# Optimization experiments

Measured on AMD Instinct MI355X. Metric: run time of the kernel, lower is better.

The kernel has to match this reference:

```python
import jax, jax.numpy as jnp
import numpy as np

N = 50000          # total residues (nodes)
E = 800000         # contact edges, avg degree 16
F_IN = 1280        # ESM embedding dim
H = 256            # hidden
L = 4              # num_layers
B = 100            # proteins in batch
MAX_NODES = 500    # residues per protein (uniform -> static to_dense_batch shape)


def setup_inputs() -> dict:
    key = jax.random.key(0)
    ks = jax.random.split(key, 16)
    s = 0.02
    inp = {
        "seq": jax.random.randint(ks[0], (N,), 0, 26),
        "edge_index": jax.random.randint(ks[1], (2, E), 0, N),
        "esm_token": jax.random.normal(ks[2], (N, F_IN), jnp.float32),
        "batch": jnp.arange(N) // MAX_NODES,
        # lin0
        "lin0_W": jax.random.normal(ks[3], (F_IN, H), jnp.float32) * s,
        "lin0_b": jnp.zeros((H,), jnp.float32),
        # WeightConv1 per layer: lin1 (root), lin2 (neighbor), lin3 (mask head)
        "wc_W1": jax.random.normal(ks[4], (L, H, H), jnp.float32) * s,
        "wc_b1": jnp.zeros((L, H), jnp.float32),
        "wc_W2": jax.random.normal(ks[5], (L, H, H), jnp.float32) * s,
        "wc_b2": jnp.zeros((L, H), jnp.float32),
        "wc_W3": jax.random.normal(ks[6], (L, H, H), jnp.float32) * s,
        "wc_b3": jnp.zeros((L, H), jnp.float32),
        # SparseConv per layer: neighbor weight + bias, root weight
        "sc_Wn": jax.random.normal(ks[7], (L, H, H), jnp.float32) * s,
        "sc_bn": jnp.zeros((L, H), jnp.float32),
        "sc_Wr": jax.random.normal(ks[8], (L, H, H), jnp.float32) * s,
    }
    return inp


def reference(seq, edge_index, esm_token, batch,
              lin0_W, lin0_b,
              wc_W1, wc_b1, wc_W2, wc_b2, wc_W3, wc_b3,
              sc_Wn, sc_bn, sc_Wr):
    src, dst = edge_index[0], edge_index[1]
    x = esm_token @ lin0_W + lin0_b              # [N, H]
    mask_val = None
    xs = []
    for i in range(L):
        # ---- WeightConv1: learned edge-conditioned node mask ----
        xm = x if mask_val is None else x * mask_val
        h_nb = xm @ wc_W2[i] + wc_b2[i]          # neighbor transform [N, H]
        agg = jax.ops.segment_sum(h_nb[src], dst, num_segments=N)
        h = jax.nn.relu(agg + xm @ wc_W1[i] + wc_b1[i])
        mask_val = jax.nn.sigmoid(h @ wc_W3[i] + wc_b3[i])   # [N, H]
        # ---- SparseConv: mask-gated sparse aggregation ----
        xg = x * mask_val
        agg2 = jax.ops.segment_sum(xg[src], dst, num_segments=N)
        x = jax.nn.relu(agg2 @ sc_Wn[i] + sc_bn[i] + x @ sc_Wr[i])
        xs.append(x)
    feat = jnp.concatenate(xs, axis=-1)          # jumping-knowledge cat [N, L*H]
    # ---- to_dense_batch ----
    counts = jax.ops.segment_sum(jnp.ones((N,), jnp.int32), batch, num_segments=B)
    starts = jnp.cumsum(counts) - counts
    pos = jnp.arange(N) - starts[batch]
    dense = jnp.zeros((B, MAX_NODES, L * H), feat.dtype).at[batch, pos].set(feat)
    node_mask = jnp.zeros((B, MAX_NODES), bool).at[batch, pos].set(True)
    return dense, node_mask
```

## Files before the change

### kernel.cpp

```cpp
#include <hip/hip_runtime.h>

#define NNODES 50000
#define HDIM 256
#define NLAYERS 4
#define NEDGES 800000
#define FIN 1280
#define LDOUT 1024

typedef _Float16 f16;
typedef __attribute__((ext_vector_type(8))) _Float16 f16x8;
typedef __attribute__((ext_vector_type(4))) _Float16 f16x4;
typedef __attribute__((ext_vector_type(4))) float f32x4;


__global__ __launch_bounds__(256) void hm_k(
    const f16*  __restrict__ aggx,
    const f16*  __restrict__ xm,
    const f16*  __restrict__ xh,
    const int*  __restrict__ deg,
    const f16*  __restrict__ WH,
    const f16*  __restrict__ W3t,
    const float* __restrict__ b2,
    const float* __restrict__ b1,
    const float* __restrict__ b3,
    f16* __restrict__ maskh,
    f16* __restrict__ xg)
{
    __shared__ f16 Hfr[16384];

    const int row0 = blockIdx.x * 64;
    const int tid = threadIdx.x;
    const int wv = tid >> 6;
    const int l = tid & 63;
    const int ak = (l >> 4) * 8;

    int arow[4]; bool av[4];
    #pragma unroll
    for (int rf = 0; rf < 4; ++rf) {
        arow[rf] = row0 + rf * 16 + (l & 15);
        av[rf] = arow[rf] < NNODES;
    }

    const f16* bp[4];
    #pragma unroll
    for (int cf = 0; cf < 4; ++cf)
        bp[cf] = WH + (size_t)(wv * 64 + cf * 16 + (l & 15)) * 512 + ak;

    f32x4 acc[4][4] = {};

    #pragma unroll
    for (int kt = 0; kt < 8; ++kt) {
        const f16* base = (kt < 4) ? aggx : xm;
        const int koff = (kt & 3) * 64 + ak;
        f16x8 af[4][2];
        #pragma unroll
        for (int rf = 0; rf < 4; ++rf)
            #pragma unroll
            for (int kb = 0; kb < 2; ++kb) {
                f16x8 v;
                #pragma unroll
                for (int i = 0; i < 8; ++i) v[i] = (f16)0.f;
                if (av[rf])
                    v = *(const f16x8*)(base + (size_t)arow[rf] * HDIM + koff + kb * 32);
                af[rf][kb] = v;
            }
        f16x8 bf[4][2];
        #pragma unroll
        for (int cf = 0; cf < 4; ++cf) {
            bf[cf][0] = *(const f16x8*)(bp[cf] + kt * 64);
            bf[cf][1] = *(const f16x8*)(bp[cf] + kt * 64 + 32);
        }
        #pragma unroll
        for (int cf = 0; cf < 4; ++cf)
            #pragma unroll
            for (int rf = 0; rf < 4; ++rf)
                #pragma unroll
                for (int kb = 0; kb < 2; ++kb)
                    acc[rf][cf] = __builtin_amdgcn_mfma_f32_16x16x32_f16(
                        af[rf][kb], bf[cf][kb], acc[rf][cf], 0, 0, 0);
    }

    #pragma unroll
    for (int rf = 0; rf < 4; ++rf) {
        #pragma unroll
        for (int j = 0; j < 4; ++j) {
            const int rowl = rf * 16 + ((l >> 4) * 4) + j;
            const int row = row0 + rowl;
            const float dv = (row < NNODES) ? (float)deg[row] : 0.f;
            #pragma unroll
            for (int cf = 0; cf < 4; ++cf) {
                const int col = wv * 64 + cf * 16 + (l & 15);
                const float h = fmaxf(acc[rf][cf][j] + dv * b2[col] + b1[col], 0.f);
                const int idx =
                    (((col >> 6) * 8 + ((col >> 5) & 1) * 4 + (rowl >> 4)) * 64
                     + ((col >> 3) & 3) * 16 + (rowl & 15)) * 8 + (col & 7);
                Hfr[idx] = (f16)h;
            }
        }
    }
    __syncthreads();

    const f16* bp3[4];
    #pragma unroll
    for (int cf = 0; cf < 4; ++cf)
        bp3[cf] = W3t + (size_t)(wv * 64 + cf * 16 + (l & 15)) * 256 + ak;

    f32x4 acc2[4][4] = {};
    #pragma unroll
    for (int kt = 0; kt < 4; ++kt) {
        f16x8 af[4][2];
        #pragma unroll
        for (int rf = 0; rf < 4; ++rf)
            #pragma unroll
            for (int kb = 0; kb < 2; ++kb)
                af[rf][kb] = *(const f16x8*)(&Hfr[((kt * 8 + kb * 4 + rf) * 64 + l) * 8]);
        f16x8 bf[4][2];
        #pragma unroll
        for (int cf = 0; cf < 4; ++cf) {
            bf[cf][0] = *(const f16x8*)(bp3[cf] + kt * 64);
            bf[cf][1] = *(const f16x8*)(bp3[cf] + kt * 64 + 32);
        }
        #pragma unroll
        for (int cf = 0; cf < 4; ++cf)
            #pragma unroll
            for (int rf = 0; rf < 4; ++rf)
                #pragma unroll
                for (int kb = 0; kb < 2; ++kb)
                    acc2[rf][cf] = __builtin_amdgcn_mfma_f32_16x16x32_f16(
                        af[rf][kb], bf[cf][kb], acc2[rf][cf], 0, 0, 0);
    }

    #pragma unroll
    for (int rf = 0; rf < 4; ++rf) {
        #pragma unroll
        for (int j = 0; j < 4; ++j) {
            const int row = row0 + rf * 16 + ((l >> 4) * 4) + j;
            if (row >= NNODES) continue;
            #pragma unroll
            for (int cf = 0; cf < 4; ++cf) {
                const int col = wv * 64 + cf * 16 + (l & 15);
                const float m = 1.f / (1.f + expf(-(acc2[rf][cf][j] + b3[col])));
                maskh[(size_t)row * HDIM + col] = (f16)m;
                xg[(size_t)row * HDIM + col] =
                    (f16)((float)xh[(size_t)row * HDIM + col] * m);
            }
        }
    }
}

__global__ __launch_bounds__(256) void cath2_k(
    const f16*  __restrict__ agg2,
    const f16*  __restrict__ xh,
    const f16*  __restrict__ Mh,
    const f16*  __restrict__ Wt,
    const float* __restrict__ bias,
    float* __restrict__ Cf, int ldc,
    f16*  __restrict__ Ch,
    f16*  __restrict__ Ch3)
{
    const int row0 = blockIdx.x * 64;
    const int tid = threadIdx.x;
    const int wv = tid >> 6;
    const int l = tid & 63;
    const int ak = (l >> 4) * 8;

    int arow[4]; bool av[4];
    #pragma unroll
    for (int rf = 0; rf < 4; ++rf) {
        arow[rf] = row0 + rf * 16 + (l & 15);
        av[rf] = arow[rf] < NNODES;
    }

    const f16* bp[4];
    #pragma unroll
    for (int cf = 0; cf < 4; ++cf)
        bp[cf] = Wt + (size_t)(wv * 64 + cf * 16 + (l & 15)) * 512 + ak;

    f32x4 acc[4][4] = {};

    #pragma unroll
    for (int kt = 0; kt < 8; ++kt) {
        const f16* base = (kt < 4) ? agg2 : xh;
        const int koff = (kt & 3) * 64 + ak;
        f16x8 af[4][2];
        #pragma unroll
        for (int rf = 0; rf < 4; ++rf)
            #pragma unroll
            for (int kb = 0; kb < 2; ++kb) {
                f16x8 v;
                #pragma unroll
                for (int i = 0; i < 8; ++i) v[i] = (f16)0.f;
                if (av[rf])
                    v = *(const f16x8*)(base + (size_t)arow[rf] * HDIM + koff + kb * 32);
                af[rf][kb] = v;
            }
        f16x8 bf[4][2];
        #pragma unroll
        for (int cf = 0; cf < 4; ++cf) {
            bf[cf][0] = *(const f16x8*)(bp[cf] + kt * 64);
            bf[cf][1] = *(const f16x8*)(bp[cf] + kt * 64 + 32);
        }
        #pragma unroll
        for (int cf = 0; cf < 4; ++cf)
            #pragma unroll
            for (int rf = 0; rf < 4; ++rf)
                #pragma unroll
                for (int kb = 0; kb < 2; ++kb)
                    acc[rf][cf] = __builtin_amdgcn_mfma_f32_16x16x32_f16(
                        af[rf][kb], bf[cf][kb], acc[rf][cf], 0, 0, 0);
    }

    __syncthreads();

    #pragma unroll
    for (int rf = 0; rf < 4; ++rf) {
        #pragma unroll
        for (int j = 0; j < 4; ++j) {
            const int row = row0 + rf * 16 + ((l >> 4) * 4) + j;
            if (row >= NNODES) continue;
            #pragma unroll
            for (int cf = 0; cf < 4; ++cf) {
                const int col = wv * 64 + cf * 16 + (l & 15);
                const float r = fmaxf(acc[rf][cf][j] + bias[col], 0.f);
                Cf[(size_t)row * ldc + col] = r;
                Ch[(size_t)row * HDIM + col] = (f16)r;
                Ch3[(size_t)row * HDIM + col] =
                    (f16)(r * (float)Mh[(size_t)row * HDIM + col]);
            }
        }
    }
}

template<int KTILES>
__global__ __launch_bounds__(256) void lin0_k(
    const float* __restrict__ A1, int lda1,
    const f16*  __restrict__ WtBase,
    f16* __restrict__ parts)
{
    constexpr int K = KTILES * 64;
    __shared__ f16 Asm[2][4096];

    const int row0 = blockIdx.x * 64;
    const int by = blockIdx.y;
    const int tid = threadIdx.x;
    const int wv = tid >> 6;
    const int l = tid & 63;

    f32x4 acc[4][4] = {};

    const int sr = tid >> 2;
    const int sc0 = (tid & 3) * 16;
    const int grow = row0 + sr;
    const bool rok = grow < NNODES;
    const int kg = by * K;
    const int lane_base0 =
        (((sc0 >> 5) * 4 + (sr >> 4)) * 64 + (sr & 15) + (((sc0 & 31) >> 3) * 16)) * 8;
    const int lane_base1 = lane_base0 + 128;

    const f16* Wsel = WtBase + (size_t)by * 256 * K;
    const f16* bp[4];
    #pragma unroll
    for (int cf = 0; cf < 4; ++cf)
        bp[cf] = Wsel + (size_t)(wv * 64 + cf * 16 + (l & 15)) * K + ((l >> 4) * 8);

    struct SReg { float4 f0, f1, f2, f3; };
    SReg RA, RB;

    auto LOAD = [&](SReg& r, int kt) {
        if (!rok) return;
        const float* p = A1 + (size_t)grow * lda1 + kg + kt * 64 + sc0;
        r.f0 = *(const float4*)(p + 0);  r.f1 = *(const float4*)(p + 4);
        r.f2 = *(const float4*)(p + 8);  r.f3 = *(const float4*)(p + 12);
    };

    auto COMMIT = [&](const SReg& r, int b) {
        f16x8 av0, av1;
        #pragma unroll
        for (int i = 0; i < 8; ++i) { av0[i] = (f16)0.f; av1[i] = (f16)0.f; }
        if (rok) {
            av0[0]=(f16)r.f0.x; av0[1]=(f16)r.f0.y; av0[2]=(f16)r.f0.z; av0[3]=(f16)r.f0.w;
            av0[4]=(f16)r.f1.x; av0[5]=(f16)r.f1.y; av0[6]=(f16)r.f1.z; av0[7]=(f16)r.f1.w;
            av1[0]=(f16)r.f2.x; av1[1]=(f16)r.f2.y; av1[2]=(f16)r.f2.z; av1[3]=(f16)r.f2.w;
            av1[4]=(f16)r.f3.x; av1[5]=(f16)r.f3.y; av1[6]=(f16)r.f3.z; av1[7]=(f16)r.f3.w;
        }
        *(f16x8*)(&Asm[b][lane_base0]) = av0;
        *(f16x8*)(&Asm[b][lane_base1]) = av1;
    };

    auto TILE = [&](int b, int kt) {
        f16x8 af[4][2];
        #pragma unroll
        for (int rf = 0; rf < 4; ++rf)
            #pragma unroll
            for (int kb = 0; kb < 2; ++kb)
                af[rf][kb] = *(const f16x8*)(&Asm[b][((kb * 4 + rf) * 64 + l) * 8]);
        f16x8 bfr[4][2];
        #pragma unroll
        for (int cf = 0; cf < 4; ++cf) {
            bfr[cf][0] = *(const f16x8*)(bp[cf] + kt * 64);
            bfr[cf][1] = *(const f16x8*)(bp[cf] + kt * 64 + 32);
        }
        #pragma unroll
        for (int cf = 0; cf < 4; ++cf)
            #pragma unroll
            for (int rf = 0; rf < 4; ++rf)
                #pragma unroll
                for (int kb = 0; kb < 2; ++kb)
                    acc[rf][cf] = __builtin_amdgcn_mfma_f32_16x16x32_f16(
                        af[rf][kb], bfr[cf][kb], acc[rf][cf], 0, 0, 0);
    };

    LOAD(RA, 0);
    COMMIT(RA, 0);
    if (KTILES > 1) LOAD(RB, 1);
    #pragma unroll
    for (int kt2 = 0; kt2 < KTILES; kt2 += 2) {
        __syncthreads();
        TILE(0, kt2);
        if (kt2 + 1 < KTILES) COMMIT(RB, 1);
        if (kt2 + 2 < KTILES) LOAD(RA, kt2 + 2);
        if (kt2 + 1 < KTILES) {
            __syncthreads();
            TILE(1, kt2 + 1);
            if (kt2 + 2 < KTILES) COMMIT(RA, 0);
            if (kt2 + 3 < KTILES) LOAD(RB, kt2 + 3);
        }
    }

    f16* Ph = parts + (size_t)by * NNODES * HDIM;
    #pragma unroll
    for (int rf = 0; rf < 4; ++rf) {
        #pragma unroll
        for (int j = 0; j < 4; ++j) {
            const int row = row0 + rf * 16 + ((l >> 4) * 4) + j;
            if (row >= NNODES) continue;
            #pragma unroll
            for (int cf = 0; cf < 4; ++cf) {
                const int col = wv * 64 + cf * 16 + (l & 15);
                Ph[(size_t)row * HDIM + col] = (f16)acc[rf][cf][j];
            }
        }
    }
}

__global__ __launch_bounds__(256) void combine4_k(
    const f16* __restrict__ parts, const float* __restrict__ b,
    f16* __restrict__ xh)
{
    const int t = blockIdx.x * 256 + threadIdx.x;
    const int row = t >> 6;
    const int c = (t & 63) * 4;
    if (row >= NNODES) return;
    const size_t NH = (size_t)NNODES * HDIM;
    const size_t off = (size_t)row * HDIM + c;
    f16x4 p0 = *(const f16x4*)(parts + off);
    f16x4 p1 = *(const f16x4*)(parts + NH + off);
    f16x4 p2 = *(const f16x4*)(parts + 2 * NH + off);
    f16x4 p3 = *(const f16x4*)(parts + 3 * NH + off);
    const float4 bb = *(const float4*)(b + c);
    f16x4 r;
    r[0] = (f16)((float)p0[0] + (float)p1[0] + (float)p2[0] + (float)p3[0] + bb.x);
    r[1] = (f16)((float)p0[1] + (float)p1[1] + (float)p2[1] + (float)p3[1] + bb.y);
    r[2] = (f16)((float)p0[2] + (float)p1[2] + (float)p2[2] + (float)p3[2] + bb.z);
    r[3] = (f16)((float)p0[3] + (float)p1[3] + (float)p2[3] + (float)p3[3] + bb.w);
    *(f16x4*)(xh + off) = r;
}

__global__ __launch_bounds__(256) void pack_all_k(
    const float* __restrict__ lin0_W,
    const float* __restrict__ W2, const float* __restrict__ W1,
    const float* __restrict__ W3,
    const float* __restrict__ Wn, const float* __restrict__ Wr,
    f16* __restrict__ dst)
{
    int idx = blockIdx.x * 256 + threadIdx.x;
    const int total = 327680 + 524288 + 262144 + 524288;
    if (idx >= total) return;
    f16* d = dst + idx;
    if (idx < 327680) {
        const int q = idx / 81920;
        int r = idx % 81920;
        const int col = r / 320, k = r % 320;
        *d = (f16)lin0_W[(size_t)(k + q * 320) * 256 + col];
        return;
    }
    idx -= 327680;
    if (idx < 524288) {
        const int i = idx / 131072;
        int r = idx % 131072;
        const int col = r / 512, k = r % 512;
        *d = (f16)(k < 256 ? W2[(size_t)i * 65536 + k * 256 + col]
                           : W1[(size_t)i * 65536 + (k - 256) * 256 + col]);
        return;
    }
    idx -= 524288;
    if (idx < 262144) {
        const int i = idx / 65536;
        int r = idx % 65536;
        const int col = r / 256, k = r % 256;
        *d = (f16)W3[(size_t)i * 65536 + k * 256 + col];
        return;
    }
    idx -= 262144;
    const int i = idx / 131072; int r = idx % 131072;
    const int col = r / 512, k = r % 512;
    *d = (f16)(k < 256 ? Wn[(size_t)i * 65536 + k * 256 + col]
                       : Wr[(size_t)i * 65536 + (k - 256) * 256 + col]);
}

__global__ __launch_bounds__(256) void count_k(
    const int* __restrict__ dstIdx, int* __restrict__ counts)
{
    const int e = blockIdx.x * 256 + threadIdx.x;
    if (e < NEDGES) atomicAdd(&counts[dstIdx[e]], 1);
}

__global__ __launch_bounds__(1024) void scan_k(
    const int* __restrict__ counts, int* __restrict__ starts)
{
    __shared__ int sm[1024];
    __shared__ int s_off;
    if (threadIdx.x == 0) s_off = 0;
    __syncthreads();
    for (int base = 0; base < NNODES; base += 1024) {
        const int i = base + threadIdx.x;
        const int v = (i < NNODES) ? counts[i] : 0;
        sm[threadIdx.x] = v;
        __syncthreads();
        for (int ofs = 1; ofs < 1024; ofs <<= 1) {
            const int t = (threadIdx.x >= ofs) ? sm[threadIdx.x - ofs] : 0;
            __syncthreads();
            sm[threadIdx.x] += t;
            __syncthreads();
        }
        const int incl = sm[threadIdx.x];
        const int off = s_off;
        if (i < NNODES) starts[i] = off + incl - v;
        __syncthreads();
        if (threadIdx.x == 1023) s_off = off + incl;
        __syncthreads();
    }
    if (threadIdx.x == 0) starts[NNODES] = s_off;
}

__global__ __launch_bounds__(256) void fillcsr_k(
    const int* __restrict__ srcIdx, const int* __restrict__ dstIdx,
    int* __restrict__ cursor, int* __restrict__ csr)
{
    const int e = blockIdx.x * 256 + threadIdx.x;
    if (e >= NEDGES) return;
    const int d = dstIdx[e];
    const int p = atomicAdd(&cursor[d], 1);
    csr[p] = srcIdx[e];
}

__global__ __launch_bounds__(256) void gather_g_k(
    const f16* __restrict__ rows, const int* __restrict__ csr,
    const int* __restrict__ starts, f16* __restrict__ outp)
{
    const int node = (blockIdx.x * 256 + threadIdx.x) >> 6;
    const int lane = threadIdx.x & 63;
    if (node >= NNODES) return;
    const int e0 = starts[node], e1 = starts[node + 1];
    float a0=0,a1=0,a2=0,a3=0, b0=0,b1=0,b2=0,b3=0;
    int e = e0;
    for (; e + 3 < e1; e += 4) {
        const int s0=csr[e], s1=csr[e+1], s2=csr[e+2], s3=csr[e+3];
        f16x4 v0 = *(const f16x4*)(rows + (size_t)s0 * HDIM + lane * 4);
        f16x4 v1 = *(const f16x4*)(rows + (size_t)s1 * HDIM + lane * 4);
        f16x4 v2 = *(const f16x4*)(rows + (size_t)s2 * HDIM + lane * 4);
        f16x4 v3 = *(const f16x4*)(rows + (size_t)s3 * HDIM + lane * 4);
        a0 += (float)v0[0] + (float)v2[0]; a1 += (float)v0[1] + (float)v2[1];
        a2 += (float)v0[2] + (float)v2[2]; a3 += (float)v0[3] + (float)v2[3];
        b0 += (float)v1[0] + (float)v3[0]; b1 += (float)v1[1] + (float)v3[1];
        b2 += (float)v1[2] + (float)v3[2]; b3 += (float)v1[3] + (float)v3[3];
    }
    for (; e < e1; ++e) {
        const int s0 = csr[e];
        f16x4 v0 = *(const f16x4*)(rows + (size_t)s0 * HDIM + lane * 4);
        a0 += (float)v0[0]; a1 += (float)v0[1]; a2 += (float)v0[2]; a3 += (float)v0[3];
    }
    f16x4 r;
    r[0] = (f16)(a0 + b0); r[1] = (f16)(a1 + b1);
    r[2] = (f16)(a2 + b2); r[3] = (f16)(a3 + b3);
    *(f16x4*)(outp + (size_t)node * HDIM + lane * 4) = r;
}

__global__ __launch_bounds__(256) void fill1_k(float* __restrict__ p, int n)
{
    const int t = blockIdx.x * 256 + threadIdx.x;
    if (t < n) p[t] = 1.0f;
}

extern "C" void kernel_launch(void* const* d_in, const int* in_sizes, int n_in,
                              void* d_out, int out_size, void* d_ws, size_t ws_size,
                              hipStream_t stream)
{
    const int*   edge   = (const int*)d_in[1];
    const int*   src    = edge;
    const int*   dst    = edge + NEDGES;
    const float* esm    = (const float*)d_in[2];
    const float* lin0_W = (const float*)d_in[4];
    const float* lin0_b = (const float*)d_in[5];
    const float* wc_W1  = (const float*)d_in[6];
    const float* wc_b1  = (const float*)d_in[7];
    const float* wc_W2  = (const float*)d_in[8];
    const float* wc_b2  = (const float*)d_in[9];
    const float* wc_W3  = (const float*)d_in[10];
    const float* wc_b3  = (const float*)d_in[11];
    const float* sc_Wn  = (const float*)d_in[12];
    const float* sc_bn  = (const float*)d_in[13];
    const float* sc_Wr  = (const float*)d_in[14];
    float* out = (float*)d_out;

    const size_t NH = (size_t)NNODES * HDIM;
    f16* parts = (f16*)d_ws;
    f16* aggx  = parts;
    f16* xg    = parts + NH;
    f16* agg2  = parts + 2 * NH;
    f16* xh    = parts + 4 * NH;
    f16* xm    = xh + NH;
    f16* maskh = xm + NH;
    f16* wpack = maskh + NH;
    f16* lin0t = wpack;
    f16* WH    = lin0t + 327680;
    f16* W3t   = WH + 524288;
    f16* WtC   = W3t + 262144;
    int* iws    = (int*)(WtC + 524288);
    int* counts = iws;
    int* starts = iws + NNODES;
    int* cursor = iws + 2 * NNODES + 1;
    int* csr    = iws + 3 * NNODES + 2;

    const dim3 blk(256);
    const int gemmGrid = (NNODES + 63) / 64;
    const int edgeGrid = (NEDGES + 255) / 256;
    const int waveGrid = (NNODES * 64) / 256;

    hipMemsetAsync(counts, 0, NNODES * sizeof(int), stream);
    count_k<<<edgeGrid, blk, 0, stream>>>(dst, counts);
    scan_k<<<1, 1024, 0, stream>>>(counts, starts);
    hipMemcpyAsync(cursor, starts, NNODES * sizeof(int),
                   hipMemcpyDeviceToDevice, stream);
    fillcsr_k<<<edgeGrid, blk, 0, stream>>>(src, dst, cursor, csr);

    pack_all_k<<<(1638400 + 255) / 256, blk, 0, stream>>>(
        lin0_W, wc_W2, wc_W1, wc_W3, sc_Wn, sc_Wr, wpack);

    lin0_k<5><<<dim3(gemmGrid, 4), blk, 0, stream>>>(esm, FIN, lin0t, parts);
    combine4_k<<<waveGrid, blk, 0, stream>>>(parts, lin0_b, xh);

    for (int i = 0; i < NLAYERS; ++i) {
        const size_t bo = (size_t)i * HDIM;
        const f16* wh = WH + (size_t)i * 131072;
        const f16* w3 = W3t + (size_t)i * 65536;
        const f16* wc = WtC + (size_t)i * 131072;
        const f16* xmtab = (i == 0) ? xh : xm;

        gather_g_k<<<waveGrid, blk, 0, stream>>>(xmtab, csr, starts, aggx);
        hm_k<<<gemmGrid, blk, 0, stream>>>(
            aggx, xmtab, xh, counts, wh, w3,
            wc_b2 + bo, wc_b1 + bo, wc_b3 + bo, maskh, xg);
        gather_g_k<<<waveGrid, blk, 0, stream>>>(xg, csr, starts, agg2);
        cath2_k<<<gemmGrid, blk, 0, stream>>>(
            agg2, xh, maskh, wc, sc_bn + bo,
            out + (size_t)i * HDIM, LDOUT, xh, xm);
    }

    const size_t maskOff = (size_t)NNODES * LDOUT;
    fill1_k<<<(NNODES + 255) / 256, blk, 0, stream>>>(out + maskOff, NNODES);
}
```

Measured before the change: 1.493 ms.

## Stage GEMM A-tiles via global_load_lds, restructure lin0, and parallelize CSR scan

Replaces the register-path A loads in the hm and cath2 GEMMs with double-buffered async global-to-LDS loads (global_load_lds). The split-K lin0 GEMM and its combine pass become a separate fp32-to-fp16 conversion of the ESM embeddings followed by a single full-K GEMM that uses the same LDS staging and fuses the bias. The single-block serial scan turns into a three-kernel block scan. The aim is to hide global latency in the GEMMs and remove the serial scan bottleneck, at the cost of an extra full fp16 copy of the input and an extra pass over it.

```diff
diff --git a/kernel.cpp b/kernel.cpp
--- a/kernel.cpp
+++ b/kernel.cpp
@@ -12,6 +12,104 @@
 typedef __attribute__((ext_vector_type(4))) _Float16 f16x4;
 typedef __attribute__((ext_vector_type(4))) float f32x4;
 
+
+__device__ __forceinline__ void gll16(const f16* g, f16* l)
+{
+    __builtin_amdgcn_global_load_lds(
+        (const __attribute__((address_space(1))) void*)g,
+        (__attribute__((address_space(3))) void*)l,
+        16, 0, 0);
+}
+
+__global__ __launch_bounds__(256) void tof16_k(
+    const float* __restrict__ in, f16* __restrict__ out)
+{
+    const long nq = (long)NNODES * FIN / 4;
+    for (long i = (long)blockIdx.x * 256 + threadIdx.x; i < nq;
+         i += (long)gridDim.x * 256) {
+        const float4 v = ((const float4*)in)[i];
+        f16x4 r;
+        r[0] = (f16)v.x; r[1] = (f16)v.y; r[2] = (f16)v.z; r[3] = (f16)v.w;
+        ((f16x4*)out)[i] = r;
+    }
+}
+
+__global__ __launch_bounds__(256) void lin0h_k(
+    const f16*  __restrict__ esmh,
+    const f16*  __restrict__ Wt,
+    const float* __restrict__ bias,
+    f16* __restrict__ xh)
+{
+    constexpr int KTILES = FIN / 64;
+    __shared__ f16 Asm[2][4096];
+
+    const int row0 = blockIdx.x * 64;
+    const int tid = threadIdx.x;
+    const int wv = tid >> 6;
+    const int l = tid & 63;
+
+    const f16* bp[4];
+    #pragma unroll
+    for (int cf = 0; cf < 4; ++cf)
+        bp[cf] = Wt + (size_t)(wv * 64 + cf * 16 + (l & 15)) * FIN + ((l >> 4) * 8);
+
+    f32x4 acc[4][4] = {};
+
+    auto STAGE = [&](int b, int kt) {
+        #pragma unroll
+        for (int i = 0; i < 2; ++i) {
+            const int r = wv * 2 + i;
+            const int rf = r & 3, kb = r >> 2;
+            int gr = row0 + rf * 16 + (l & 15);
+            gr = (gr < NNODES) ? gr : (NNODES - 1);
+            gll16(esmh + (size_t)gr * FIN + kt * 64 + kb * 32 + ((l >> 4) * 8),
+                  &Asm[b][r * 512]);
+        }
+    };
+
+    STAGE(0, 0);
+    int cur = 0;
+    #pragma unroll
+    for (int kt = 0; kt < KTILES; ++kt) {
+        __syncthreads();
+        if (kt + 1 < KTILES) STAGE(cur ^ 1, kt + 1);
+        f16x8 af[4][2];
+        #pragma unroll
+        for (int rf = 0; rf < 4; ++rf)
+            #pragma unroll
+            for (int kb = 0; kb < 2; ++kb)
+                af[rf][kb] = *(const f16x8*)(&Asm[cur][((kb * 4 + rf) * 64 + l) * 8]);
+        f16x8 bf[4][2];
+        #pragma unroll
+        for (int cf = 0; cf < 4; ++cf) {
+            bf[cf][0] = *(const f16x8*)(bp[cf] + kt * 64);
+            bf[cf][1] = *(const f16x8*)(bp[cf] + kt * 64 + 32);
+        }
+        #pragma unroll
+        for (int cf = 0; cf < 4; ++cf)
+            #pragma unroll
+            for (int rf = 0; rf < 4; ++rf)
+                #pragma unroll
+                for (int kb = 0; kb < 2; ++kb)
+                    acc[rf][cf] = __builtin_amdgcn_mfma_f32_16x16x32_f16(
+                        af[rf][kb], bf[cf][kb], acc[rf][cf], 0, 0, 0);
+        cur ^= 1;
+    }
+
+    #pragma unroll
+    for (int rf = 0; rf < 4; ++rf) {
+        #pragma unroll
+        for (int j = 0; j < 4; ++j) {
+            const int row = row0 + rf * 16 + ((l >> 4) * 4) + j;
+            if (row >= NNODES) continue;
+            #pragma unroll
+            for (int cf = 0; cf < 4; ++cf) {
+                const int col = wv * 64 + cf * 16 + (l & 15);
+                xh[(size_t)row * HDIM + col] = (f16)(acc[rf][cf][j] + bias[col]);
+            }
+        }
+    }
+}
 
 __global__ __launch_bounds__(256) void hm_k(
     const f16*  __restrict__ aggx,
@@ -26,44 +124,47 @@
     f16* __restrict__ maskh,
     f16* __restrict__ xg)
 {
-    __shared__ f16 Hfr[16384];
+    __shared__ f16 lds[16384];
+    f16 (*Asm)[4096] = (f16(*)[4096])lds;
 
     const int row0 = blockIdx.x * 64;
     const int tid = threadIdx.x;
     const int wv = tid >> 6;
     const int l = tid & 63;
-    const int ak = (l >> 4) * 8;
-
-    int arow[4]; bool av[4];
-    #pragma unroll
-    for (int rf = 0; rf < 4; ++rf) {
-        arow[rf] = row0 + rf * 16 + (l & 15);
-        av[rf] = arow[rf] < NNODES;
-    }
 
     const f16* bp[4];
     #pragma unroll
     for (int cf = 0; cf < 4; ++cf)
-        bp[cf] = WH + (size_t)(wv * 64 + cf * 16 + (l & 15)) * 512 + ak;
+        bp[cf] = WH + (size_t)(wv * 64 + cf * 16 + (l & 15)) * 512 + ((l >> 4) * 8);
 
     f32x4 acc[4][4] = {};
 
+    auto STAGE = [&](int b, int kt) {
+        const f16* base = (kt < 4) ? aggx : xm;
+        const int ko = (kt & 3) * 64;
+        #pragma unroll
+        for (int i = 0; i < 2; ++i) {
+            const int r = wv * 2 + i;
+            const int rf = r & 3, kb = r >> 2;
+            int gr = row0 + rf * 16 + (l & 15);
+            gr = (gr < NNODES) ? gr : (NNODES - 1);
+            gll16(base + (size_t)gr * HDIM + ko + kb * 32 + ((l >> 4) * 8),
+                  &Asm[b][r * 512]);
+        }
+    };
+
+    STAGE(0, 0);
+    int cur = 0;
     #pragma unroll
     for (int kt = 0; kt < 8; ++kt) {
-        const f16* base = (kt < 4) ? aggx : xm;
-        const int koff = (kt & 3) * 64 + ak;
+        __syncthreads();
+        if (kt + 1 < 8) STAGE(cur ^ 1, kt + 1);
         f16x8 af[4][2];
         #pragma unroll
         for (int rf = 0; rf < 4; ++rf)
             #pragma unroll
-            for (int kb = 0; kb < 2; ++kb) {
-                f16x8 v;
-                #pragma unroll
-                for (int i = 0; i < 8; ++i) v[i] = (f16)0.f;
-                if (av[rf])
-                    v = *(const f16x8*)(base + (size_t)arow[rf] * HDIM + koff + kb * 32);
-                af[rf][kb] = v;
-            }
+            for (int kb = 0; kb < 2; ++kb)
+                af[rf][kb] = *(const f16x8*)(&Asm[cur][((kb * 4 + rf) * 64 + l) * 8]);
         f16x8 bf[4][2];
         #pragma unroll
         for (int cf = 0; cf < 4; ++cf) {
@@ -78,7 +179,9 @@
                 for (int kb = 0; kb < 2; ++kb)
                     acc[rf][cf] = __builtin_amdgcn_mfma_f32_16x16x32_f16(
                         af[rf][kb], bf[cf][kb], acc[rf][cf], 0, 0, 0);
-    }
+        cur ^= 1;
+    }
+    __syncthreads();
 
     #pragma unroll
     for (int rf = 0; rf < 4; ++rf) {
@@ -94,7 +197,7 @@
                 const int idx =
                     (((col >> 6) * 8 + ((col >> 5) & 1) * 4 + (rowl >> 4)) * 64
                      + ((col >> 3) & 3) * 16 + (rowl & 15)) * 8 + (col & 7);
-                Hfr[idx] = (f16)h;
+                lds[idx] = (f16)h;
             }
         }
     }
@@ -103,7 +206,7 @@
     const f16* bp3[4];
     #pragma unroll
     for (int cf = 0; cf < 4; ++cf)
-        bp3[cf] = W3t + (size_t)(wv * 64 + cf * 16 + (l & 15)) * 256 + ak;
+        bp3[cf] = W3t + (size_t)(wv * 64 + cf * 16 + (l & 15)) * 256 + ((l >> 4) * 8);
 
     f32x4 acc2[4][4] = {};
     #pragma unroll
@@ -113,7 +216,7 @@
         for (int rf = 0; rf < 4; ++rf)
             #pragma unroll
             for (int kb = 0; kb < 2; ++kb)
-                af[rf][kb] = *(const f16x8*)(&Hfr[((kt * 8 + kb * 4 + rf) * 64 + l) * 8]);
+                af[rf][kb] = *(const f16x8*)(&lds[((kt * 8 + kb * 4 + rf) * 64 + l) * 8]);
         f16x8 bf[4][2];
         #pragma unroll
         for (int cf = 0; cf < 4; ++cf) {
@@ -158,42 +261,46 @@
     f16*  __restrict__ Ch,
     f16*  __restrict__ Ch3)
 {
+    __shared__ f16 Asm[2][4096];
+
     const int row0 = blockIdx.x * 64;
     const int tid = threadIdx.x;
     const int wv = tid >> 6;
     const int l = tid & 63;
-    const int ak = (l >> 4) * 8;
-
-    int arow[4]; bool av[4];
-    #pragma unroll
-    for (int rf = 0; rf < 4; ++rf) {
-        arow[rf] = row0 + rf * 16 + (l & 15);
-        av[rf] = arow[rf] < NNODES;
-    }
 
     const f16* bp[4];
     #pragma unroll
     for (int cf = 0; cf < 4; ++cf)
-        bp[cf] = Wt + (size_t)(wv * 64 + cf * 16 + (l & 15)) * 512 + ak;
+        bp[cf] = Wt + (size_t)(wv * 64 + cf * 16 + (l & 15)) * 512 + ((l >> 4) * 8);
 
     f32x4 acc[4][4] = {};
 
+    auto STAGE = [&](int b, int kt) {
+        const f16* base = (kt < 4) ? agg2 : xh;
+        const int ko = (kt & 3) * 64;
+        #pragma unroll
+        for (int i = 0; i < 2; ++i) {
+            const int r = wv * 2 + i;
+            const int rf = r & 3, kb = r >> 2;
+            int gr = row0 + rf * 16 + (l & 15);
+            gr = (gr < NNODES) ? gr : (NNODES - 1);
+            gll16(base + (size_t)gr * HDIM + ko + kb * 32 + ((l >> 4) * 8),
+                  &Asm[b][r * 512]);
+        }
+    };
+
+    STAGE(0, 0);
+    int cur = 0;
     #pragma unroll
     for (int kt = 0; kt < 8; ++kt) {
-        const f16* base = (kt < 4) ? agg2 : xh;
-        const int koff = (kt & 3) * 64 + ak;
+        __syncthreads();
+        if (kt + 1 < 8) STAGE(cur ^ 1, kt + 1);
         f16x8 af[4][2];
         #pragma unroll
         for (int rf = 0; rf < 4; ++rf)
             #pragma unroll
-            for (int kb = 0; kb < 2; ++kb) {
-                f16x8 v;
-                #pragma unroll
-                for (int i = 0; i < 8; ++i) v[i] = (f16)0.f;
-                if (av[rf])
-                    v = *(const f16x8*)(base + (size_t)arow[rf] * HDIM + koff + kb * 32);
-                af[rf][kb] = v;
-            }
+            for (int kb = 0; kb < 2; ++kb)
+                af[rf][kb] = *(const f16x8*)(&Asm[cur][((kb * 4 + rf) * 64 + l) * 8]);
         f16x8 bf[4][2];
         #pragma unroll
         for (int cf = 0; cf < 4; ++cf) {
@@ -208,9 +315,8 @@
                 for (int kb = 0; kb < 2; ++kb)
                     acc[rf][cf] = __builtin_amdgcn_mfma_f32_16x16x32_f16(
                         af[rf][kb], bf[cf][kb], acc[rf][cf], 0, 0, 0);
-    }
-
-    __syncthreads();
+        cur ^= 1;
+    }
 
     #pragma unroll
     for (int rf = 0; rf < 4; ++rf) {
@@ -231,141 +337,6 @@
     }
 }
 
-template<int KTILES>
-__global__ __launch_bounds__(256) void lin0_k(
-    const float* __restrict__ A1, int lda1,
-    const f16*  __restrict__ WtBase,
-    f16* __restrict__ parts)
-{
-    constexpr int K = KTILES * 64;
-    __shared__ f16 Asm[2][4096];
-
-    const int row0 = blockIdx.x * 64;
-    const int by = blockIdx.y;
-    const int tid = threadIdx.x;
-    const int wv = tid >> 6;
-    const int l = tid & 63;
-
-    f32x4 acc[4][4] = {};
-
-    const int sr = tid >> 2;
-    const int sc0 = (tid & 3) * 16;
-    const int grow = row0 + sr;
-    const bool rok = grow < NNODES;
-    const int kg = by * K;
-    const int lane_base0 =
-        (((sc0 >> 5) * 4 + (sr >> 4)) * 64 + (sr & 15) + (((sc0 & 31) >> 3) * 16)) * 8;
-    const int lane_base1 = lane_base0 + 128;
-
-    const f16* Wsel = WtBase + (size_t)by * 256 * K;
-    const f16* bp[4];
-    #pragma unroll
-    for (int cf = 0; cf < 4; ++cf)
-        bp[cf] = Wsel + (size_t)(wv * 64 + cf * 16 + (l & 15)) * K + ((l >> 4) * 8);
-
-    struct SReg { float4 f0, f1, f2, f3; };
-    SReg RA, RB;
-
-    auto LOAD = [&](SReg& r, int kt) {
-        if (!rok) return;
-        const float* p = A1 + (size_t)grow * lda1 + kg + kt * 64 + sc0;
-        r.f0 = *(const float4*)(p + 0);  r.f1 = *(const float4*)(p + 4);
-        r.f2 = *(const float4*)(p + 8);  r.f3 = *(const float4*)(p + 12);
-    };
-
-    auto COMMIT = [&](const SReg& r, int b) {
-        f16x8 av0, av1;
-        #pragma unroll
-        for (int i = 0; i < 8; ++i) { av0[i] = (f16)0.f; av1[i] = (f16)0.f; }
-        if (rok) {
-            av0[0]=(f16)r.f0.x; av0[1]=(f16)r.f0.y; av0[2]=(f16)r.f0.z; av0[3]=(f16)r.f0.w;
-            av0[4]=(f16)r.f1.x; av0[5]=(f16)r.f1.y; av0[6]=(f16)r.f1.z; av0[7]=(f16)r.f1.w;
-            av1[0]=(f16)r.f2.x; av1[1]=(f16)r.f2.y; av1[2]=(f16)r.f2.z; av1[3]=(f16)r.f2.w;
-            av1[4]=(f16)r.f3.x; av1[5]=(f16)r.f3.y; av1[6]=(f16)r.f3.z; av1[7]=(f16)r.f3.w;
-        }
-        *(f16x8*)(&Asm[b][lane_base0]) = av0;
-        *(f16x8*)(&Asm[b][lane_base1]) = av1;
-    };
-
-    auto TILE = [&](int b, int kt) {
-        f16x8 af[4][2];
-        #pragma unroll
-        for (int rf = 0; rf < 4; ++rf)
-            #pragma unroll
-            for (int kb = 0; kb < 2; ++kb)
-                af[rf][kb] = *(const f16x8*)(&Asm[b][((kb * 4 + rf) * 64 + l) * 8]);
-        f16x8 bfr[4][2];
-        #pragma unroll
-        for (int cf = 0; cf < 4; ++cf) {
-            bfr[cf][0] = *(const f16x8*)(bp[cf] + kt * 64);
-            bfr[cf][1] = *(const f16x8*)(bp[cf] + kt * 64 + 32);
-        }
-        #pragma unroll
-        for (int cf = 0; cf < 4; ++cf)
-            #pragma unroll
-            for (int rf = 0; rf < 4; ++rf)
-                #pragma unroll
-                for (int kb = 0; kb < 2; ++kb)
-                    acc[rf][cf] = __builtin_amdgcn_mfma_f32_16x16x32_f16(
-                        af[rf][kb], bfr[cf][kb], acc[rf][cf], 0, 0, 0);
-    };
-
-    LOAD(RA, 0);
-    COMMIT(RA, 0);
-    if (KTILES > 1) LOAD(RB, 1);
-    #pragma unroll
-    for (int kt2 = 0; kt2 < KTILES; kt2 += 2) {
-        __syncthreads();
-        TILE(0, kt2);
-        if (kt2 + 1 < KTILES) COMMIT(RB, 1);
-        if (kt2 + 2 < KTILES) LOAD(RA, kt2 + 2);
-        if (kt2 + 1 < KTILES) {
-            __syncthreads();
-            TILE(1, kt2 + 1);
-            if (kt2 + 2 < KTILES) COMMIT(RA, 0);
-            if (kt2 + 3 < KTILES) LOAD(RB, kt2 + 3);
-        }
-    }
-
-    f16* Ph = parts + (size_t)by * NNODES * HDIM;
-    #pragma unroll
-    for (int rf = 0; rf < 4; ++rf) {
-        #pragma unroll
-        for (int j = 0; j < 4; ++j) {
-            const int row = row0 + rf * 16 + ((l >> 4) * 4) + j;
-            if (row >= NNODES) continue;
-            #pragma unroll
-            for (int cf = 0; cf < 4; ++cf) {
-                const int col = wv * 64 + cf * 16 + (l & 15);
-                Ph[(size_t)row * HDIM + col] = (f16)acc[rf][cf][j];
-            }
-        }
-    }
-}
-
-__global__ __launch_bounds__(256) void combine4_k(
-    const f16* __restrict__ parts, const float* __restrict__ b,
-    f16* __restrict__ xh)
-{
-    const int t = blockIdx.x * 256 + threadIdx.x;
-    const int row = t >> 6;
-    const int c = (t & 63) * 4;
-    if (row >= NNODES) return;
-    const size_t NH = (size_t)NNODES * HDIM;
-    const size_t off = (size_t)row * HDIM + c;
-    f16x4 p0 = *(const f16x4*)(parts + off);
-    f16x4 p1 = *(const f16x4*)(parts + NH + off);
-    f16x4 p2 = *(const f16x4*)(parts + 2 * NH + off);
-    f16x4 p3 = *(const f16x4*)(parts + 3 * NH + off);
-    const float4 bb = *(const float4*)(b + c);
-    f16x4 r;
-    r[0] = (f16)((float)p0[0] + (float)p1[0] + (float)p2[0] + (float)p3[0] + bb.x);
-    r[1] = (f16)((float)p0[1] + (float)p1[1] + (float)p2[1] + (float)p3[1] + bb.y);
-    r[2] = (f16)((float)p0[2] + (float)p1[2] + (float)p2[2] + (float)p3[2] + bb.z);
-    r[3] = (f16)((float)p0[3] + (float)p1[3] + (float)p2[3] + (float)p3[3] + bb.w);
-    *(f16x4*)(xh + off) = r;
-}
-
 __global__ __launch_bounds__(256) void pack_all_k(
     const float* __restrict__ lin0_W,
     const float* __restrict__ W2, const float* __restrict__ W1,
@@ -378,10 +349,8 @@
     if (idx >= total) return;
     f16* d = dst + idx;
     if (idx < 327680) {
-        const int q = idx / 81920;
-        int r = idx % 81920;
-        const int col = r / 320, k = r % 320;
-        *d = (f16)lin0_W[(size_t)(k + q * 320) * 256 + col];
+        const int col = idx / 1280, k = idx % 1280;
+        *d = (f16)lin0_W[(size_t)k * 256 + col];
         return;
     }
     idx -= 327680;
@@ -415,32 +384,48 @@
     if (e < NEDGES) atomicAdd(&counts[dstIdx[e]], 1);
 }
 
-__global__ __launch_bounds__(1024) void scan_k(
-    const int* __restrict__ counts, int* __restrict__ starts)
-{
-    __shared__ int sm[1024];
-    __shared__ int s_off;
-    if (threadIdx.x == 0) s_off = 0;
+__global__ __launch_bounds__(256) void scan1_k(
+    const int* __restrict__ counts, int* __restrict__ starts,
+    int* __restrict__ bsums)
+{
+    __shared__ int sm[256];
+    const int i = blockIdx.x * 256 + threadIdx.x;
+    const int v = (i < NNODES) ? counts[i] : 0;
+    sm[threadIdx.x] = v;
     __syncthreads();
-    for (int base = 0; base < NNODES; base += 1024) {
-        const int i = base + threadIdx.x;
-        const int v = (i < NNODES) ? counts[i] : 0;
-        sm[threadIdx.x] = v;
-        __syncthreads();
-        for (int ofs = 1; ofs < 1024; ofs <<= 1) {
-            const int t = (threadIdx.x >= ofs) ? sm[threadIdx.x - ofs] : 0;
-            __syncthreads();
-            sm[threadIdx.x] += t;
-            __syncthreads();
-        }
-        const int incl = sm[threadIdx.x];
-        const int off = s_off;
-        if (i < NNODES) starts[i] = off + incl - v;
-        __syncthreads();
-        if (threadIdx.x == 1023) s_off = off + incl;
-        __syncthreads();
-    }
-    if (threadIdx.x == 0) starts[NNODES] = s_off;
+    #pragma unroll
+    for (int ofs = 1; ofs < 256; ofs <<= 1) {
+        const int t = (threadIdx.x >= ofs) ? sm[threadIdx.x - ofs] : 0;
+        __syncthreads();
+        sm[threadIdx.x] += t;
+        __syncthreads();
+    }
+    if (i < NNODES) starts[i] = sm[threadIdx.x] - v;
+    if (threadIdx.x == 255) bsums[blockIdx.x] = sm[255];
+}
+
+__global__ __launch_bounds__(256) void scan2_k(int* __restrict__ bsums, int nb)
+{
+    __shared__ int sm[256];
+    const int v = (threadIdx.x < nb) ? bsums[threadIdx.x] : 0;
+    sm[threadIdx.x] = v;
+    __syncthreads();
+    #pragma unroll
+    for (int ofs = 1; ofs < 256; ofs <<= 1) {
+        const int t = (threadIdx.x >= ofs) ? sm[threadIdx.x - ofs] : 0;
+        __syncthreads();
+        sm[threadIdx.x] += t;
+        __syncthreads();
+    }
+    if (threadIdx.x < nb) bsums[threadIdx.x] = sm[threadIdx.x] - v;
+}
+
+__global__ __launch_bounds__(256) void scan3_k(
+    const int* __restrict__ bsums, int* __restrict__ starts)
+{
+    const int i = blockIdx.x * 256 + threadIdx.x;
+    if (i < NNODES) starts[i] += bsums[blockIdx.x];
+    if (i == 0) starts[NNODES] = NEDGES;
 }
 
 __global__ __launch_bounds__(256) void fillcsr_k(
@@ -514,14 +499,14 @@
     float* out = (float*)d_out;
 
     const size_t NH = (size_t)NNODES * HDIM;
-    f16* parts = (f16*)d_ws;
-    f16* aggx  = parts;
-    f16* xg    = parts + NH;
-    f16* agg2  = parts + 2 * NH;
-    f16* xh    = parts + 4 * NH;
+    f16* aggx  = (f16*)d_ws;
+    f16* xg    = aggx + NH;
+    f16* agg2  = xg + NH;
+    f16* xh    = agg2 + NH;
     f16* xm    = xh + NH;
     f16* maskh = xm + NH;
-    f16* wpack = maskh + NH;
+    f16* esmh  = maskh + NH;
+    f16* wpack = esmh + (size_t)NNODES * FIN;
     f16* lin0t = wpack;
     f16* WH    = lin0t + 327680;
     f16* W3t   = WH + 524288;
@@ -531,24 +516,28 @@
     int* starts = iws + NNODES;
     int* cursor = iws + 2 * NNODES + 1;
     int* csr    = iws + 3 * NNODES + 2;
+    int* bsums  = csr + NEDGES;
 
     const dim3 blk(256);
     const int gemmGrid = (NNODES + 63) / 64;
     const int edgeGrid = (NEDGES + 255) / 256;
     const int waveGrid = (NNODES * 64) / 256;
+    const int scanGrid = (NNODES + 255) / 256;
 
     hipMemsetAsync(counts, 0, NNODES * sizeof(int), stream);
     count_k<<<edgeGrid, blk, 0, stream>>>(dst, counts);
-    scan_k<<<1, 1024, 0, stream>>>(counts, starts);
+    scan1_k<<<scanGrid, blk, 0, stream>>>(counts, starts, bsums);
+    scan2_k<<<1, blk, 0, stream>>>(bsums, scanGrid);
+    scan3_k<<<scanGrid, blk, 0, stream>>>(bsums, starts);
     hipMemcpyAsync(cursor, starts, NNODES * sizeof(int),
                    hipMemcpyDeviceToDevice, stream);
     fillcsr_k<<<edgeGrid, blk, 0, stream>>>(src, dst, cursor, csr);
 
     pack_all_k<<<(1638400 + 255) / 256, blk, 0, stream>>>(
         lin0_W, wc_W2, wc_W1, wc_W3, sc_Wn, sc_Wr, wpack);
-
-    lin0_k<5><<<dim3(gemmGrid, 4), blk, 0, stream>>>(esm, FIN, lin0t, parts);
-    combine4_k<<<waveGrid, blk, 0, stream>>>(parts, lin0_b, xh);
+    tof16_k<<<2048, blk, 0, stream>>>(esm, esmh);
+
+    lin0h_k<<<gemmGrid, blk, 0, stream>>>(esmh, lin0t, lin0_b, xh);
 
     for (int i = 0; i < NLAYERS; ++i) {
         const size_t bo = (size_t)i * HDIM;
```

Result: faster. 1.351 ms (-9.5%).
